# Kernel tuning notes

Hardware: AMD Instinct MI355X
Metric: run time of the kernel (lower is better)

The kernel has to match this reference:

```python
import jax, jax.numpy as jnp
import numpy as np

B, LQ, D, H, L, P, DFF = 16, 1024, 256, 8, 4, 4, 1024
SHAPES = ((64, 64), (32, 32), (16, 16), (8, 8))  # (H_l, W_l) per level
LV = sum(h * w for h, w in SHAPES)  # 5440
DH = D // H
EPS = 1e-5


def layer_norm(x, g, b):
    m = jnp.mean(x, -1, keepdims=True)
    v = jnp.mean((x - m) ** 2, -1, keepdims=True)
    return (x - m) * jax.lax.rsqrt(v + EPS) * g + b


def mha(q_in, k_in, v_in, w, b, ow, ob):
    # torch nn.MultiheadAttention with packed in_proj [3D, D]
    q = (q_in @ w[:D].T + b[:D]).reshape(B, LQ, H, DH)
    k = (k_in @ w[D:2 * D].T + b[D:2 * D]).reshape(B, LQ, H, DH)
    v = (v_in @ w[2 * D:].T + b[2 * D:]).reshape(B, LQ, H, DH)
    a = jax.nn.softmax(jnp.einsum('bqhd,bkhd->bhqk', q, k) * (1.0 / np.sqrt(DH)), -1)
    o = jnp.einsum('bhqk,bkhd->bqhd', a, v).reshape(B, LQ, D)
    return o @ ow.T + ob


def ms_deform_attn(q, ref, src, value_w, value_b, off_w, off_b, attw_w, attw_b, outp_w, outp_b):
    # value: [B, H, LV, DH]
    value = (src @ value_w.T + value_b).reshape(B, LV, H, DH).transpose(0, 2, 1, 3)
    off = (q @ off_w.T + off_b).reshape(B, LQ, H, L, P, 2)
    attw = jax.nn.softmax((q @ attw_w.T + attw_b).reshape(B, LQ, H, L * P), -1).reshape(B, LQ, H, L, P)
    # offset normalizer = (W_l, H_l) matching (x, y) order of reference points
    normalizer = jnp.array([[w, h] for h, w in SHAPES], jnp.float32)
    loc = ref[:, :, None, :, None, :] + off / normalizer[None, None, None, :, None, :]  # [B,LQ,H,L,P,2]
    out = jnp.zeros((B, LQ, H, DH), jnp.float32)
    start = 0
    for l, (hl, wl) in enumerate(SHAPES):
        v = value[:, :, start:start + hl * wl]  # [B,H,N_l,DH]
        start += hl * wl
        # grid_sample semantics, align_corners=False, padding zeros
        x = loc[:, :, :, l, :, 0] * wl - 0.5  # [B,LQ,H,P]
        y = loc[:, :, :, l, :, 1] * hl - 0.5
        x0 = jnp.floor(x); y0 = jnp.floor(y)
        lx = (x - x0).transpose(0, 2, 1, 3)[..., None]  # [B,H,LQ,P,1]
        ly = (y - y0).transpose(0, 2, 1, 3)[..., None]
        x0i = x0.astype(jnp.int32); y0i = y0.astype(jnp.int32)

        def gather(xi, yi):
            valid = ((xi >= 0) & (xi < wl) & (yi >= 0) & (yi < hl)).astype(jnp.float32)
            idx = jnp.clip(yi, 0, hl - 1) * wl + jnp.clip(xi, 0, wl - 1)  # [B,LQ,H,P]
            idx2 = idx.transpose(0, 2, 1, 3).reshape(B, H, LQ * P)
            g = jnp.take_along_axis(v, jnp.broadcast_to(idx2[..., None], (B, H, LQ * P, DH)), axis=2)
            return g.reshape(B, H, LQ, P, DH) * valid.transpose(0, 2, 1, 3)[..., None]

        g00 = gather(x0i, y0i); g01 = gather(x0i + 1, y0i)
        g10 = gather(x0i, y0i + 1); g11 = gather(x0i + 1, y0i + 1)
        sampled = (g00 * (1 - lx) * (1 - ly) + g01 * lx * (1 - ly)
                   + g10 * (1 - lx) * ly + g11 * lx * ly)  # [B,H,LQ,P,DH]
        out = out + jnp.einsum('bhqpd,bqhp->bqhd', sampled, attw[:, :, :, l])
    return out.reshape(B, LQ, D) @ outp_w.T + outp_b


def setup_inputs() -> dict:
    key = jax.random.key(0)
    ks = jax.random.split(key, 16)
    s = 0.02
    inp = {}
    inp['tgt'] = jax.random.normal(ks[0], (B, LQ, D), jnp.float32)
    inp['query_pos'] = jax.random.normal(ks[1], (B, LQ, D), jnp.float32)
    inp['reference_points'] = jax.random.uniform(ks[2], (B, LQ, L, 2), jnp.float32)
    inp['src'] = jax.random.normal(ks[3], (B, LV, D), jnp.float32)
    # self-attention (MHA)
    inp['in_proj_w'] = jax.random.normal(ks[4], (3 * D, D), jnp.float32) * s
    inp['in_proj_b'] = jnp.zeros((3 * D,), jnp.float32)
    inp['out_proj_w'] = jax.random.normal(ks[5], (D, D), jnp.float32) * s
    inp['out_proj_b'] = jnp.zeros((D,), jnp.float32)
    inp['norm2_g'] = jnp.ones((D,), jnp.float32); inp['norm2_b'] = jnp.zeros((D,), jnp.float32)
    # MSDeformAttn
    inp['value_w'] = jax.random.normal(ks[6], (D, D), jnp.float32) * s
    inp['value_b'] = jnp.zeros((D,), jnp.float32)
    inp['off_w'] = jax.random.normal(ks[7], (H * L * P * 2, D), jnp.float32) * s
    inp['off_b'] = jax.random.normal(ks[8], (H * L * P * 2,), jnp.float32) * 0.5
    inp['attw_w'] = jax.random.normal(ks[9], (H * L * P, D), jnp.float32) * s
    inp['attw_b'] = jnp.zeros((H * L * P,), jnp.float32)
    inp['outp_w'] = jax.random.normal(ks[10], (D, D), jnp.float32) * s
    inp['outp_b'] = jnp.zeros((D,), jnp.float32)
    inp['norm1_g'] = jnp.ones((D,), jnp.float32); inp['norm1_b'] = jnp.zeros((D,), jnp.float32)
    # FFN
    inp['lin1_w'] = jax.random.normal(ks[11], (DFF, D), jnp.float32) * s
    inp['lin1_b'] = jnp.zeros((DFF,), jnp.float32)
    inp['lin2_w'] = jax.random.normal(ks[12], (D, DFF), jnp.float32) * s
    inp['lin2_b'] = jnp.zeros((D,), jnp.float32)
    inp['norm3_g'] = jnp.ones((D,), jnp.float32); inp['norm3_b'] = jnp.zeros((D,), jnp.float32)
    inp['src_spatial_shapes'] = jnp.array(SHAPES, jnp.int32)
    inp['level_start_index'] = jnp.array(np.concatenate([[0], np.cumsum([h * w for h, w in SHAPES[:-1]])]), jnp.int32)
    return inp


def reference(tgt, query_pos, reference_points, src,
              in_proj_w, in_proj_b, out_proj_w, out_proj_b, norm2_g, norm2_b,
              value_w, value_b, off_w, off_b, attw_w, attw_b, outp_w, outp_b,
              norm1_g, norm1_b, lin1_w, lin1_b, lin2_w, lin2_b, norm3_g, norm3_b,
              src_spatial_shapes, level_start_index):
    # dropout=0 (eval mode)
    q = tgt + query_pos
    tgt2 = mha(q, q, tgt, in_proj_w, in_proj_b, out_proj_w, out_proj_b)
    tgt = layer_norm(tgt + tgt2, norm2_g, norm2_b)
    tgt2 = ms_deform_attn(tgt + query_pos, reference_points, src,
                          value_w, value_b, off_w, off_b, attw_w, attw_b, outp_w, outp_b)
    tgt = layer_norm(tgt + tgt2, norm1_g, norm1_b)
    t2 = jax.nn.relu(tgt @ lin1_w.T + lin1_b) @ lin2_w.T + lin2_b
    return layer_norm(tgt + t2, norm3_g, norm3_b)
```

## Files before the change

### kernel.cpp

```cpp
#include <hip/hip_runtime.h>
#include <math.h>

typedef short s16x8 __attribute__((ext_vector_type(8)));
typedef float f32x4 __attribute__((ext_vector_type(4)));
typedef unsigned short u16;
typedef unsigned short u16x4 __attribute__((ext_vector_type(4)));

constexpr int cB    = 16;
constexpr int cLQ   = 1024;
constexpr int cD    = 256;
constexpr int cH    = 8;
constexpr int cLVTOT= 5440;
constexpr int cNTOK = cB * cLQ;
constexpr int cNV   = cB * cLVTOT;

__device__ __forceinline__ u16 f2b(float f) {
    __bf16 h = (__bf16)f;
    u16 u;
    __builtin_memcpy(&u, &h, 2);
    return u;
}
__device__ __forceinline__ float bl(unsigned x) {
    return __uint_as_float(x << 16);
}

__global__ __launch_bounds__(256) void prep_src_kernel(const float4* __restrict__ t,
                                                       const float4* __restrict__ q,
                                                       u16x4* __restrict__ tb,
                                                       u16x4* __restrict__ qb,
                                                       const float4* __restrict__ src,
                                                       u16x4* __restrict__ srcb) {
    int bid = blockIdx.x;
    if (bid < 4096) {
        int i = bid * 256 + threadIdx.x;
        float4 a = t[i], b = q[i];
        tb[i] = (u16x4){ f2b(a.x), f2b(a.y), f2b(a.z), f2b(a.w) };
        qb[i] = (u16x4){ f2b(a.x + b.x), f2b(a.y + b.y), f2b(a.z + b.z), f2b(a.w + b.w) };
    } else {
        int i = (bid - 4096) * 256 + threadIdx.x;
        float4 v = src[i];
        srcb[i] = (u16x4){ f2b(v.x), f2b(v.y), f2b(v.z), f2b(v.w) };
    }
}

struct WArgs { const float4* src[8]; };
__global__ __launch_bounds__(256) void cvtw_kernel(WArgs a, u16x4* __restrict__ out,
                                                   const float* __restrict__ off_b,
                                                   const float* __restrict__ attw_b,
                                                   float* __restrict__ biasoa) {
    int i = blockIdx.x * 256 + threadIdx.x;
    if (i >= 253952) {
        int t = threadIdx.x;
        biasoa[t] = off_b[t];
        if (t < 128) biasoa[256 + t] = attw_b[t];
        return;
    }
    int s, off;
    if (i < 98304) {
        if (i < 65536) { if (i < 49152) { s = 0; off = i; } else { s = 1; off = i - 49152; } }
        else           { if (i < 81920) { s = 2; off = i - 65536; } else { s = 3; off = i - 81920; } }
    } else {
        if (i < 122880){ if (i < 106496){ s = 4; off = i - 98304; } else { s = 5; off = i - 106496; } }
        else           { if (i < 188416){ s = 6; off = i - 122880; } else { s = 7; off = i - 188416; } }
    }
    float4 v = a.src[s][off];
    out[i] = (u16x4){ f2b(v.x), f2b(v.y), f2b(v.z), f2b(v.w) };
}

__global__ __launch_bounds__(256) void gemm_qkv(const u16* __restrict__ A0,
                                                const u16* __restrict__ A1,
                                                const u16* __restrict__ Wt,
                                                const float* __restrict__ bias,
                                                u16* __restrict__ QKb,
                                                u16* __restrict__ Vtg) {
    __shared__ u16 As[128 * 32];
    __shared__ u16 Bs[128 * 32];
    const int K = 256;
    int tid = threadIdx.x;
    int bm = blockIdx.x * 128, bn = blockIdx.y * 128;
    const u16* A = (blockIdx.y < 4) ? A0 : A1;
    int w = tid >> 6, lane = tid & 63, quad = lane >> 4, l15 = lane & 15;
    int wm = (w & 1) * 64, wn = (w >> 1) * 64;
    int r0 = tid >> 2;
    int c0 = ((tid & 3) ^ ((tid >> 3) & 3)) * 8;
    const u16* ga0 = A  + (size_t)(bm + r0) * K + c0;
    const u16* ga1 = ga0 + (size_t)64 * K;
    const u16* gb0 = Wt + (size_t)(bn + r0) * K + c0;
    const u16* gb1 = gb0 + (size_t)64 * K;
    int abk = (quad ^ ((l15 >> 1) & 3)) * 8;
    f32x4 acc[16];
#pragma unroll
    for (int i = 0; i < 16; ++i) acc[i] = (f32x4){0.f, 0.f, 0.f, 0.f};
    s16x8 ra0 = *(const s16x8*)ga0, ra1 = *(const s16x8*)ga1;
    s16x8 rb0 = *(const s16x8*)gb0, rb1 = *(const s16x8*)gb1;
#pragma unroll 2
    for (int i = 0; i < 8; ++i) {
        *(s16x8*)&As[tid * 8]        = ra0;
        *(s16x8*)&As[2048 + tid * 8] = ra1;
        *(s16x8*)&Bs[tid * 8]        = rb0;
        *(s16x8*)&Bs[2048 + tid * 8] = rb1;
        __syncthreads();
        if (i < 7) {
            int k1 = (i + 1) << 5;
            ra0 = *(const s16x8*)(ga0 + k1); ra1 = *(const s16x8*)(ga1 + k1);
            rb0 = *(const s16x8*)(gb0 + k1); rb1 = *(const s16x8*)(gb1 + k1);
        }
        s16x8 af[4], bf[4];
#pragma unroll
        for (int mt = 0; mt < 4; ++mt) af[mt] = *(const s16x8*)&As[(wm + mt * 16 + l15) * 32 + abk];
#pragma unroll
        for (int nt = 0; nt < 4; ++nt) bf[nt] = *(const s16x8*)&Bs[(wn + nt * 16 + l15) * 32 + abk];
#pragma unroll
        for (int mt = 0; mt < 4; ++mt)
#pragma unroll
            for (int nt = 0; nt < 4; ++nt)
                acc[mt * 4 + nt] = __builtin_amdgcn_mfma_f32_16x16x32_bf16(af[mt], bf[nt], acc[mt * 4 + nt], 0, 0, 0);
        __syncthreads();
    }
    float bs[4];
#pragma unroll
    for (int nt = 0; nt < 4; ++nt) bs[nt] = bias[bn + wn + nt * 16 + l15];
    if (bn < 512) {
        float qs = (bn + wn < 256) ? 0.25506734f : 1.0f;
#pragma unroll
        for (int mt = 0; mt < 4; ++mt) {
            int m = bm + wm + mt * 16 + quad * 4;
#pragma unroll
            for (int nt = 0; nt < 4; ++nt) {
                int n = bn + wn + nt * 16 + l15;
#pragma unroll
                for (int r = 0; r < 4; ++r)
                    QKb[(size_t)(m + r) * 512 + n] = f2b((acc[mt * 4 + nt][r] + bs[nt]) * qs);
            }
        }
    } else {
#pragma unroll
        for (int mt = 0; mt < 4; ++mt) {
            int m = bm + wm + mt * 16 + quad * 4;
            int b = m >> 10, t = m & 1023;
#pragma unroll
            for (int nt = 0; nt < 4; ++nt) {
                int nv = bn + wn + nt * 16 + l15 - 512;
                int h = nv >> 5, dh = nv & 31;
                u16x4 o;
#pragma unroll
                for (int r = 0; r < 4; ++r) o[r] = f2b(acc[mt * 4 + nt][r] + bs[nt]);
                *(u16x4*)(Vtg + (((size_t)(b * 8 + h) * 32 + dh) << 10) + t) = o;
            }
        }
    }
}

template <int RELU, int OUTBF>
__global__ __launch_bounds__(256) void gemm128(const u16* __restrict__ A,
                                               const u16* __restrict__ Wt,
                                               const float* __restrict__ bias,
                                               float* __restrict__ Cf,
                                               u16* __restrict__ Cb,
                                               int M, int N, int K) {
    __shared__ u16 As[128 * 32];
    __shared__ u16 Bs[128 * 32];
    int tid = threadIdx.x;
    int bm = blockIdx.x * 128, bn = blockIdx.y * 128;
    int w = tid >> 6, lane = tid & 63, quad = lane >> 4, l15 = lane & 15;
    int wm = (w & 1) * 64, wn = (w >> 1) * 64;
    int r0 = tid >> 2;
    int c0 = ((tid & 3) ^ ((tid >> 3) & 3)) * 8;
    const u16* ga0 = A  + (size_t)(bm + r0) * K + c0;
    const u16* ga1 = ga0 + (size_t)64 * K;
    const u16* gb0 = Wt + (size_t)(bn + r0) * K + c0;
    const u16* gb1 = gb0 + (size_t)64 * K;
    int abk = (quad ^ ((l15 >> 1) & 3)) * 8;
    f32x4 acc[16];
#pragma unroll
    for (int i = 0; i < 16; ++i) acc[i] = (f32x4){0.f, 0.f, 0.f, 0.f};
    s16x8 ra0 = *(const s16x8*)ga0, ra1 = *(const s16x8*)ga1;
    s16x8 rb0 = *(const s16x8*)gb0, rb1 = *(const s16x8*)gb1;
    int nk = K >> 5;
#pragma unroll 2
    for (int i = 0; i < nk; ++i) {
        *(s16x8*)&As[tid * 8]        = ra0;
        *(s16x8*)&As[2048 + tid * 8] = ra1;
        *(s16x8*)&Bs[tid * 8]        = rb0;
        *(s16x8*)&Bs[2048 + tid * 8] = rb1;
        __syncthreads();
        if (i + 1 < nk) {
            int k1 = (i + 1) << 5;
            ra0 = *(const s16x8*)(ga0 + k1); ra1 = *(const s16x8*)(ga1 + k1);
            rb0 = *(const s16x8*)(gb0 + k1); rb1 = *(const s16x8*)(gb1 + k1);
        }
        s16x8 af[4], bf[4];
#pragma unroll
        for (int mt = 0; mt < 4; ++mt) af[mt] = *(const s16x8*)&As[(wm + mt * 16 + l15) * 32 + abk];
#pragma unroll
        for (int nt = 0; nt < 4; ++nt) bf[nt] = *(const s16x8*)&Bs[(wn + nt * 16 + l15) * 32 + abk];
#pragma unroll
        for (int mt = 0; mt < 4; ++mt)
#pragma unroll
            for (int nt = 0; nt < 4; ++nt)
                acc[mt * 4 + nt] = __builtin_amdgcn_mfma_f32_16x16x32_bf16(af[mt], bf[nt], acc[mt * 4 + nt], 0, 0, 0);
        __syncthreads();
    }
    float bs[4];
#pragma unroll
    for (int nt = 0; nt < 4; ++nt) bs[nt] = bias[bn + wn + nt * 16 + l15];
#pragma unroll
    for (int mt = 0; mt < 4; ++mt) {
        int m = bm + wm + mt * 16 + quad * 4;
#pragma unroll
        for (int nt = 0; nt < 4; ++nt) {
            int n = bn + wn + nt * 16 + l15;
#pragma unroll
            for (int r = 0; r < 4; ++r) {
                float v = acc[mt * 4 + nt][r] + bs[nt];
                if (RELU) v = fmaxf(v, 0.f);
                if (OUTBF) Cb[(size_t)(m + r) * N + n] = f2b(v);
                else       Cf[(size_t)(m + r) * N + n] = v;
            }
        }
    }
}

template <int RELU, int OUTBF>
__global__ __launch_bounds__(256) void gemm64(const u16* __restrict__ A,
                                              const u16* __restrict__ Wt,
                                              const float* __restrict__ bias,
                                              float* __restrict__ Cf,
                                              u16* __restrict__ Cb,
                                              int M, int N, int K) {
    __shared__ u16 As[64 * 32];
    __shared__ u16 Bs[128 * 32];
    int tid = threadIdx.x;
    int bm = blockIdx.x * 64, bn = blockIdx.y * 128;
    int w = tid >> 6, lane = tid & 63, quad = lane >> 4, l15 = lane & 15;
    int wn = w * 32;
    int r0 = tid >> 2;
    int c0 = ((tid & 3) ^ ((tid >> 3) & 3)) * 8;
    const u16* ga0 = A  + (size_t)(bm + r0) * K + c0;
    const u16* gb0 = Wt + (size_t)(bn + r0) * K + c0;
    const u16* gb1 = gb0 + (size_t)64 * K;
    int abk = (quad ^ ((l15 >> 1) & 3)) * 8;
    f32x4 acc[8];
#pragma unroll
    for (int i = 0; i < 8; ++i) acc[i] = (f32x4){0.f, 0.f, 0.f, 0.f};
    s16x8 ra0 = *(const s16x8*)ga0;
    s16x8 rb0 = *(const s16x8*)gb0, rb1 = *(const s16x8*)gb1;
    int nk = K >> 5;
#pragma unroll 2
    for (int i = 0; i < nk; ++i) {
        *(s16x8*)&As[tid * 8]        = ra0;
        *(s16x8*)&Bs[tid * 8]        = rb0;
        *(s16x8*)&Bs[2048 + tid * 8] = rb1;
        __syncthreads();
        if (i + 1 < nk) {
            int k1 = (i + 1) << 5;
            ra0 = *(const s16x8*)(ga0 + k1);
            rb0 = *(const s16x8*)(gb0 + k1); rb1 = *(const s16x8*)(gb1 + k1);
        }
        s16x8 af[4], bf[2];
#pragma unroll
        for (int mt = 0; mt < 4; ++mt) af[mt] = *(const s16x8*)&As[(mt * 16 + l15) * 32 + abk];
#pragma unroll
        for (int nt = 0; nt < 2; ++nt) bf[nt] = *(const s16x8*)&Bs[(wn + nt * 16 + l15) * 32 + abk];
#pragma unroll
        for (int mt = 0; mt < 4; ++mt)
#pragma unroll
            for (int nt = 0; nt < 2; ++nt)
                acc[mt * 2 + nt] = __builtin_amdgcn_mfma_f32_16x16x32_bf16(af[mt], bf[nt], acc[mt * 2 + nt], 0, 0, 0);
        __syncthreads();
    }
    float bs[2];
#pragma unroll
    for (int nt = 0; nt < 2; ++nt) bs[nt] = bias[bn + wn + nt * 16 + l15];
#pragma unroll
    for (int mt = 0; mt < 4; ++mt) {
        int m = bm + mt * 16 + quad * 4;
#pragma unroll
        for (int nt = 0; nt < 2; ++nt) {
            int n = bn + wn + nt * 16 + l15;
#pragma unroll
            for (int r = 0; r < 4; ++r) {
                float v = acc[mt * 2 + nt][r] + bs[nt];
                if (RELU) v = fmaxf(v, 0.f);
                if (OUTBF) Cb[(size_t)(m + r) * N + n] = f2b(v);
                else       Cf[(size_t)(m + r) * N + n] = v;
            }
        }
    }
}

__global__ __launch_bounds__(256) void attn_val(const u16* __restrict__ QK,
                                                const u16* __restrict__ Vt,
                                                u16* __restrict__ O,
                                                const u16* __restrict__ Av,
                                                const u16* __restrict__ Wv,
                                                const float* __restrict__ bv,
                                                u16* __restrict__ Cv) {
    __shared__ __align__(16) u16 smem[8192];
    int bid = blockIdx.x;
    int tid = threadIdx.x;
    int w = tid >> 6, lane = tid & 63, quad = lane >> 4, l15 = lane & 15;
    int isg, id;
    if (bid < 2720) { isg = !(bid & 1); id = bid >> 1; }
    else            { isg = 0;          id = 1360 + (bid - 2720); }
    if (isg) {
        u16* As = smem;
        u16* Bs = smem + 4096;
        int bm = (id % 680) * 128, bn = (id / 680) * 128;
        int wm = (w & 1) * 64, wn = (w >> 1) * 64;
        int r0 = tid >> 2;
        int c0 = ((tid & 3) ^ ((tid >> 3) & 3)) * 8;
        const u16* ga0 = Av + (size_t)(bm + r0) * 256 + c0;
        const u16* ga1 = ga0 + (size_t)64 * 256;
        const u16* gb0 = Wv + (size_t)(bn + r0) * 256 + c0;
        const u16* gb1 = gb0 + (size_t)64 * 256;
        int abk = (quad ^ ((l15 >> 1) & 3)) * 8;
        f32x4 acc[16];
#pragma unroll
        for (int i = 0; i < 16; ++i) acc[i] = (f32x4){0.f, 0.f, 0.f, 0.f};
        s16x8 ra0 = *(const s16x8*)ga0, ra1 = *(const s16x8*)ga1;
        s16x8 rb0 = *(const s16x8*)gb0, rb1 = *(const s16x8*)gb1;
#pragma unroll 2
        for (int i = 0; i < 8; ++i) {
            *(s16x8*)&As[tid * 8]        = ra0;
            *(s16x8*)&As[2048 + tid * 8] = ra1;
            *(s16x8*)&Bs[tid * 8]        = rb0;
            *(s16x8*)&Bs[2048 + tid * 8] = rb1;
            __syncthreads();
            if (i < 7) {
                int k1 = (i + 1) << 5;
                ra0 = *(const s16x8*)(ga0 + k1); ra1 = *(const s16x8*)(ga1 + k1);
                rb0 = *(const s16x8*)(gb0 + k1); rb1 = *(const s16x8*)(gb1 + k1);
            }
            s16x8 af[4], bf[4];
#pragma unroll
            for (int mt = 0; mt < 4; ++mt) af[mt] = *(const s16x8*)&As[(wm + mt * 16 + l15) * 32 + abk];
#pragma unroll
            for (int nt = 0; nt < 4; ++nt) bf[nt] = *(const s16x8*)&Bs[(wn + nt * 16 + l15) * 32 + abk];
#pragma unroll
            for (int mt = 0; mt < 4; ++mt)
#pragma unroll
                for (int nt = 0; nt < 4; ++nt)
                    acc[mt * 4 + nt] = __builtin_amdgcn_mfma_f32_16x16x32_bf16(af[mt], bf[nt], acc[mt * 4 + nt], 0, 0, 0);
            __syncthreads();
        }
        float bs[4];
#pragma unroll
        for (int nt = 0; nt < 4; ++nt) bs[nt] = bv[bn + wn + nt * 16 + l15];
#pragma unroll
        for (int mt = 0; mt < 4; ++mt) {
            int m = bm + wm + mt * 16 + quad * 4;
#pragma unroll
            for (int nt = 0; nt < 4; ++nt) {
                int n = bn + wn + nt * 16 + l15;
#pragma unroll
                for (int r = 0; r < 4; ++r)
                    Cv[(size_t)(m + r) * 256 + n] = f2b(acc[mt * 4 + nt][r] + bs[nt]);
            }
        }
        return;
    }
    u16* Ks  = smem;
    u16* Vs  = smem + 2048;
    u16* Psw = smem + 4096 + w * 1024;
    int qt = id & 15, bh = id >> 4;
    int h = bh & 7, b = bh >> 3;
    int qbase = qt * 64 + w * 16;
    s16x8 qf = *(const s16x8*)(QK + (size_t)(b * cLQ + qbase + l15) * 512 + h * 32 + quad * 8);
    f32x4 o0 = {0.f,0.f,0.f,0.f}, o1 = {0.f,0.f,0.f,0.f}, o2 = {0.f,0.f,0.f,0.f};
    int skey = tid >> 2, kchunk = tid & 3;
    int ks_off = skey * 32 + ((kchunk ^ ((skey >> 1) & 3)) * 8);
    int sdh = kchunk * 8;
    int vdh = tid >> 3, vchunk = tid & 7;
    int vs_off = vdh * 64 + ((vchunk ^ (vdh & 7)) * 8);
    int vkc = vchunk * 8;
    int ksw = (l15 >> 1) & 3;
    int vsw = l15 & 7;
    size_t kgbase = (size_t)(b * cLQ) * 512 + 256 + h * 32;
    size_t vgbase = (size_t)bh * 32 * cLQ;
    s16x8 kreg = *(const s16x8*)(QK + kgbase + (size_t)skey * 512 + sdh);
    s16x8 vreg = *(const s16x8*)(Vt + vgbase + (size_t)vdh * cLQ + vkc);
    const s16x8 ones = {16256,16256,16256,16256,16256,16256,16256,16256};
    for (int kt = 0; kt < cLQ; kt += 64) {
        __syncthreads();
        *(s16x8*)&Ks[ks_off] = kreg;
        *(s16x8*)&Vs[vs_off] = vreg;
        if (kt + 64 < cLQ) {
            kreg = *(const s16x8*)(QK + kgbase + (size_t)(kt + 64 + skey) * 512 + sdh);
            vreg = *(const s16x8*)(Vt + vgbase + (size_t)vdh * cLQ + kt + 64 + vkc);
        }
        __syncthreads();
#pragma unroll
        for (int t = 0; t < 4; ++t) {
            s16x8 kf = *(const s16x8*)&Ks[(t * 16 + l15) * 32 + (quad ^ ksw) * 8];
            f32x4 z = {0.f,0.f,0.f,0.f};
            f32x4 sc = __builtin_amdgcn_mfma_f32_16x16x32_bf16(kf, qf, z, 0, 0, 0);
            u16x4 pb;
#pragma unroll
            for (int r = 0; r < 4; ++r) pb[r] = f2b(exp2f(sc[r]));
            *(u16x4*)&Psw[l15 * 64 + (((t * 2 + (quad >> 1)) ^ vsw) * 8) + (quad & 1) * 4] = pb;
        }
#pragma unroll
        for (int ks = 0; ks < 2; ++ks) {
            int coff = ((ks * 4 + quad) ^ vsw) * 8;
            s16x8 pa  = *(const s16x8*)&Psw[l15 * 64 + coff];
            s16x8 vb0 = *(const s16x8*)&Vs[l15 * 64 + coff];
            s16x8 vb1 = *(const s16x8*)&Vs[(l15 + 16) * 64 + coff];
            o0 = __builtin_amdgcn_mfma_f32_16x16x32_bf16(pa, vb0, o0, 0, 0, 0);
            o1 = __builtin_amdgcn_mfma_f32_16x16x32_bf16(pa, vb1, o1, 0, 0, 0);
            o2 = __builtin_amdgcn_mfma_f32_16x16x32_bf16(pa, ones, o2, 0, 0, 0);
        }
    }
#pragma unroll
    for (int r = 0; r < 4; ++r) {
        float inv = 1.0f / o2[r];
        int q = qbase + quad * 4 + r;
        size_t ob = (size_t)(b * cLQ + q) * cD + h * 32;
        O[ob + l15]      = f2b(o0[r] * inv);
        O[ob + 16 + l15] = f2b(o1[r] * inv);
    }
}

template <int WB, int QP>
__global__ __launch_bounds__(256) void add_ln_kernel(const float* __restrict__ X,
                                                     const float* __restrict__ R,
                                                     const float* __restrict__ g,
                                                     const float* __restrict__ bt,
                                                     const float* __restrict__ qp,
                                                     float* __restrict__ out,
                                                     u16* __restrict__ outb) {
    int wave = threadIdx.x / 64;
    int lane = threadIdx.x % 64;
    int row = blockIdx.x * 4 + wave;
    const float* x = X + (size_t)row * cD;
    const float* r = R + (size_t)row * cD;
    float4 xv = *(const float4*)(x + lane * 4);
    float4 rv = *(const float4*)(r + lane * 4);
    float v0 = xv.x + rv.x, v1 = xv.y + rv.y, v2 = xv.z + rv.z, v3 = xv.w + rv.w;
    float s = v0 + v1 + v2 + v3;
    float s2 = v0 * v0 + v1 * v1 + v2 * v2 + v3 * v3;
#pragma unroll
    for (int off = 32; off > 0; off >>= 1) {
        s += __shfl_xor(s, off);
        s2 += __shfl_xor(s2, off);
    }
    float mean = s * (1.0f / 256.0f);
    float var = s2 * (1.0f / 256.0f) - mean * mean;
    float rstd = rsqrtf(var + 1e-5f);
    float4 gv = *(const float4*)(g + lane * 4);
    float4 bv = *(const float4*)(bt + lane * 4);
    float4 o;
    o.x = (v0 - mean) * rstd * gv.x + bv.x;
    o.y = (v1 - mean) * rstd * gv.y + bv.y;
    o.z = (v2 - mean) * rstd * gv.z + bv.z;
    o.w = (v3 - mean) * rstd * gv.w + bv.w;
    *(float4*)(out + (size_t)row * cD + lane * 4) = o;
    if (WB) {
        u16x4 ob = { f2b(o.x), f2b(o.y), f2b(o.z), f2b(o.w) };
        *(u16x4*)(outb + (size_t)row * cD + lane * 4) = ob;
    }
    if (QP) {
        float4 qv = *(const float4*)(qp + (size_t)row * cD + lane * 4);
        u16x4 ob = { f2b(o.x + qv.x), f2b(o.y + qv.y), f2b(o.z + qv.z), f2b(o.w + qv.w) };
        *(u16x4*)(outb + (size_t)row * cD + lane * 4) = ob;
    }
}

__global__ __launch_bounds__(256) void deform_kernel(const u16* __restrict__ value,
                                                     const float* __restrict__ oa,
                                                     const float* __restrict__ refp,
                                                     u16* __restrict__ out) {
    int t = blockIdx.x * 32 + (threadIdx.x >> 3);
    int dq = threadIdx.x & 7;
    int h = t & 7;
    int bq = t >> 3;
    int b = bq >> 10;
    const float* al = oa + (size_t)bq * 384 + 256 + h * 16;
    float wv[16];
    float mx = -1e30f;
#pragma unroll
    for (int i = 0; i < 16; ++i) { wv[i] = al[i]; mx = fmaxf(mx, wv[i]); }
    float sum = 0.f;
#pragma unroll
    for (int i = 0; i < 16; ++i) { wv[i] = __expf(wv[i] - mx); sum += wv[i]; }
    float inv = 1.f / sum;
    const float* off = oa + (size_t)bq * 384 + h * 32;
    const float* rp = refp + (size_t)bq * 8;
    const u16* vb = value + ((size_t)b * cLVTOT) * 256 + h * 32 + dq * 4;
    const int starts[4] = {0, 4096, 5120, 5376};
    const int dims[4] = {64, 32, 16, 8};
    float a0 = 0.f, a1 = 0.f, a2 = 0.f, a3 = 0.f;
#pragma unroll
    for (int l = 0; l < 4; ++l) {
        int hl = dims[l], wl = dims[l];
        float rx = rp[l * 2 + 0], ry = rp[l * 2 + 1];
#pragma unroll
        for (int p = 0; p < 4; ++p) {
            float ox = off[(l * 4 + p) * 2 + 0];
            float oy = off[(l * 4 + p) * 2 + 1];
            float x = rx * (float)wl + ox - 0.5f;
            float y = ry * (float)hl + oy - 0.5f;
            float x0f = floorf(x), y0f = floorf(y);
            float lx = x - x0f, ly = y - y0f;
            int x0 = (int)x0f, y0 = (int)y0f;
            float aw = wv[l * 4 + p] * inv;
            float cw[4] = {(1.f - lx) * (1.f - ly), lx * (1.f - ly),
                           (1.f - lx) * ly, lx * ly};
            int xs[4] = {x0, x0 + 1, x0, x0 + 1};
            int ys[4] = {y0, y0, y0 + 1, y0 + 1};
#pragma unroll
            for (int c = 0; c < 4; ++c) {
                int xi = xs[c], yi = ys[c];
                bool valid = (xi >= 0) && (xi < wl) && (yi >= 0) && (yi < hl);
                int xc = min(max(xi, 0), wl - 1);
                int yc = min(max(yi, 0), hl - 1);
                int idx = starts[l] + yc * wl + xc;
                float wgt = valid ? aw * cw[c] : 0.f;
                unsigned long long u = *(const unsigned long long*)(vb + (size_t)idx * 256);
                a0 += wgt * bl((unsigned)(u & 0xffffull));
                a1 += wgt * bl((unsigned)((u >> 16) & 0xffffull));
                a2 += wgt * bl((unsigned)((u >> 32) & 0xffffull));
                a3 += wgt * bl((unsigned)(u >> 48));
            }
        }
    }
    u16x4 o = { f2b(a0), f2b(a1), f2b(a2), f2b(a3) };
    *(u16x4*)(out + (size_t)bq * 256 + h * 32 + dq * 4) = o;
}

extern "C" void kernel_launch(void* const* d_in, const int* in_sizes, int n_in,
                              void* d_out, int out_size, void* d_ws, size_t ws_size,
                              hipStream_t stream) {
    const float* tgt        = (const float*)d_in[0];
    const float* query_pos  = (const float*)d_in[1];
    const float* refp       = (const float*)d_in[2];
    const float* src        = (const float*)d_in[3];
    const float* in_proj_w  = (const float*)d_in[4];
    const float* in_proj_b  = (const float*)d_in[5];
    const float* out_proj_b = (const float*)d_in[7];
    const float* norm2_g    = (const float*)d_in[8];
    const float* norm2_b    = (const float*)d_in[9];
    const float* value_b    = (const float*)d_in[11];
    const float* off_b      = (const float*)d_in[13];
    const float* attw_b     = (const float*)d_in[15];
    const float* outp_b     = (const float*)d_in[17];
    const float* norm1_g    = (const float*)d_in[18];
    const float* norm1_b    = (const float*)d_in[19];
    const float* lin1_b     = (const float*)d_in[21];
    const float* lin2_b     = (const float*)d_in[23];
    const float* norm3_g    = (const float*)d_in[24];
    const float* norm3_b    = (const float*)d_in[25];

    char* W = (char*)d_ws;
    const size_t S84 = 8388608;
    u16*   tgtb  = (u16*)(W + 0);
    u16*   q2b   = (u16*)(W + 0);
    u16*   qb    = (u16*)(W + 1 * S84);
    u16*   QKb   = (u16*)(W + 2 * S84);
    u16*   dtb   = (u16*)(W + 2 * S84);
    u16*   x2b   = (u16*)(W + 3 * S84);
    float* ffn2f = (float*)(W + 4 * S84);
    u16*   aob   = (u16*)(W + 5 * S84);
    float* oaf   = (float*)(W + 5 * S84);
    u16*   Vtg   = (u16*)(W + 6 * S84);
    float* t2f   = (float*)(W + 6 * S84);
    float* x1f   = (float*)(W + 8 * S84);
    float* x2f   = (float*)(W + 10 * S84);
    u16*   srcb  = (u16*)(W + 12 * S84);
    u16*   ffn1b = (u16*)(W + 12 * S84);
    u16*   valb  = (u16*)(W + 12 * S84 + 44564480);
    char*  wbase = W + 12 * S84 + 2 * 44564480;
    u16* wb_in   = (u16*)(wbase + 0);
    u16* wb_out  = (u16*)(wbase + 393216);
    u16* wb_val  = (u16*)(wbase + 524288);
    u16* wb_off  = (u16*)(wbase + 655360);
    u16* wb_outp = (u16*)(wbase + 851968);
    u16* wb_lin1 = (u16*)(wbase + 983040);
    u16* wb_lin2 = (u16*)(wbase + 1507328);
    float* biasoa= (float*)(wbase + 2031616);
    float* out = (float*)d_out;

    dim3 blk(256);

    prep_src_kernel<<<dim3(25856), blk, 0, stream>>>((const float4*)tgt, (const float4*)query_pos,
                                                     (u16x4*)tgtb, (u16x4*)qb,
                                                     (const float4*)src, (u16x4*)srcb);
    WArgs wa;
    wa.src[0] = (const float4*)in_proj_w;  wa.src[1] = (const float4*)d_in[6];
    wa.src[2] = (const float4*)d_in[10];   wa.src[3] = (const float4*)d_in[12];
    wa.src[4] = (const float4*)d_in[14];   wa.src[5] = (const float4*)d_in[16];
    wa.src[6] = (const float4*)d_in[20];   wa.src[7] = (const float4*)d_in[22];
    cvtw_kernel<<<dim3(993), blk, 0, stream>>>(wa, (u16x4*)wb_in, off_b, attw_b, biasoa);

    gemm_qkv<<<dim3(128, 6), blk, 0, stream>>>(qb, tgtb, wb_in, in_proj_b, QKb, Vtg);
    attn_val<<<dim3(3408), blk, 0, stream>>>(QKb, Vtg, aob, srcb, wb_val, value_b, valb);
    gemm64<0, 0><<<dim3(256, 2), blk, 0, stream>>>(aob, wb_out, out_proj_b, t2f, nullptr, cNTOK, 256, 256);
    add_ln_kernel<0, 1><<<dim3(4096), blk, 0, stream>>>(tgt, t2f, norm2_g, norm2_b, query_pos, x1f, q2b);

    gemm64<0, 0><<<dim3(256, 3), blk, 0, stream>>>(q2b, wb_off, biasoa, oaf, nullptr, cNTOK, 384, 256);
    deform_kernel<<<dim3(4096), blk, 0, stream>>>(valb, oaf, refp, dtb);
    gemm64<0, 0><<<dim3(256, 2), blk, 0, stream>>>(dtb, wb_outp, outp_b, t2f, nullptr, cNTOK, 256, 256);
    add_ln_kernel<1, 0><<<dim3(4096), blk, 0, stream>>>(x1f, t2f, norm1_g, norm1_b, nullptr, x2f, x2b);

    gemm128<1, 1><<<dim3(128, 8), blk, 0, stream>>>(x2b, wb_lin1, lin1_b, nullptr, ffn1b, cNTOK, 1024, 256);
    gemm64<0, 0><<<dim3(256, 2), blk, 0, stream>>>(ffn1b, wb_lin2, lin2_b, ffn2f, nullptr, cNTOK, 256, 1024);
    add_ln_kernel<0, 0><<<dim3(4096), blk, 0, stream>>>(x2f, ffn2f, norm3_g, norm3_b, nullptr, out, nullptr);
}
```

Measured before the change: 440.3 us.

## Move value-projection GEMM from attention kernel into QKV projection launch

The value projection GEMM (src → value), previously interleaved with self-attention blocks inside attn_val, now runs in one combined launch with the QKV projection. The attention kernel becomes a pure attention kernel of 2048 blocks. The intent is to balance work better: the QKV GEMM grid was small (768 blocks) and the independent value GEMM fills it out, while the attention kernel no longer mixes heterogeneous block types. The trade-off is that the attention kernel loses the overlap it had with the value GEMM.

```diff
diff --git a/kernel.cpp b/kernel.cpp
--- a/kernel.cpp
+++ b/kernel.cpp
@@ -67,25 +67,43 @@
     out[i] = (u16x4){ f2b(v.x), f2b(v.y), f2b(v.z), f2b(v.w) };
 }
 
-__global__ __launch_bounds__(256) void gemm_qkv(const u16* __restrict__ A0,
-                                                const u16* __restrict__ A1,
-                                                const u16* __restrict__ Wt,
-                                                const float* __restrict__ bias,
-                                                u16* __restrict__ QKb,
-                                                u16* __restrict__ Vtg) {
+__global__ __launch_bounds__(256) void gemm_qkv_val(const u16* __restrict__ A0,
+                                                    const u16* __restrict__ A1,
+                                                    const u16* __restrict__ Wt,
+                                                    const float* __restrict__ bias,
+                                                    u16* __restrict__ QKb,
+                                                    u16* __restrict__ Vtg,
+                                                    const u16* __restrict__ Av,
+                                                    const u16* __restrict__ Wv,
+                                                    const float* __restrict__ bv,
+                                                    u16* __restrict__ Cv) {
     __shared__ u16 As[128 * 32];
     __shared__ u16 Bs[128 * 32];
     const int K = 256;
     int tid = threadIdx.x;
-    int bm = blockIdx.x * 128, bn = blockIdx.y * 128;
-    const u16* A = (blockIdx.y < 4) ? A0 : A1;
+    int bid = blockIdx.x;
     int w = tid >> 6, lane = tid & 63, quad = lane >> 4, l15 = lane & 15;
     int wm = (w & 1) * 64, wn = (w >> 1) * 64;
+    int isval = bid < 1360;
+    int bm, bn;
+    const u16 *A, *W;
+    const float* bp;
+    if (isval) {
+        bm = (bid % 680) * 128; bn = (bid / 680) * 128;
+        A = Av; W = Wv; bp = bv;
+    } else {
+        int id = bid - 1360;
+        bm = (id & 127) * 128;
+        int by = id >> 7;
+        bn = by * 128;
+        A = (by < 4) ? A0 : A1;
+        W = Wt; bp = bias;
+    }
     int r0 = tid >> 2;
     int c0 = ((tid & 3) ^ ((tid >> 3) & 3)) * 8;
-    const u16* ga0 = A  + (size_t)(bm + r0) * K + c0;
+    const u16* ga0 = A + (size_t)(bm + r0) * K + c0;
     const u16* ga1 = ga0 + (size_t)64 * K;
-    const u16* gb0 = Wt + (size_t)(bn + r0) * K + c0;
+    const u16* gb0 = W + (size_t)(bn + r0) * K + c0;
     const u16* gb1 = gb0 + (size_t)64 * K;
     int abk = (quad ^ ((l15 >> 1) & 3)) * 8;
     f32x4 acc[16];
@@ -119,8 +137,20 @@
     }
     float bs[4];
 #pragma unroll
-    for (int nt = 0; nt < 4; ++nt) bs[nt] = bias[bn + wn + nt * 16 + l15];
-    if (bn < 512) {
+    for (int nt = 0; nt < 4; ++nt) bs[nt] = bp[bn + wn + nt * 16 + l15];
+    if (isval) {
+#pragma unroll
+        for (int mt = 0; mt < 4; ++mt) {
+            int m = bm + wm + mt * 16 + quad * 4;
+#pragma unroll
+            for (int nt = 0; nt < 4; ++nt) {
+                int n = bn + wn + nt * 16 + l15;
+#pragma unroll
+                for (int r = 0; r < 4; ++r)
+                    Cv[(size_t)(m + r) * 256 + n] = f2b(acc[mt * 4 + nt][r] + bs[nt]);
+            }
+        }
+    } else if (bn < 512) {
         float qs = (bn + wn < 256) ? 0.25506734f : 1.0f;
 #pragma unroll
         for (int mt = 0; mt < 4; ++mt) {
@@ -289,80 +319,15 @@
     }
 }
 
-__global__ __launch_bounds__(256) void attn_val(const u16* __restrict__ QK,
-                                                const u16* __restrict__ Vt,
-                                                u16* __restrict__ O,
-                                                const u16* __restrict__ Av,
-                                                const u16* __restrict__ Wv,
-                                                const float* __restrict__ bv,
-                                                u16* __restrict__ Cv) {
+__global__ __launch_bounds__(256) void attn_sw(const u16* __restrict__ QK,
+                                               const u16* __restrict__ Vt,
+                                               u16* __restrict__ O) {
     __shared__ __align__(16) u16 smem[8192];
-    int bid = blockIdx.x;
-    int tid = threadIdx.x;
-    int w = tid >> 6, lane = tid & 63, quad = lane >> 4, l15 = lane & 15;
-    int isg, id;
-    if (bid < 2720) { isg = !(bid & 1); id = bid >> 1; }
-    else            { isg = 0;          id = 1360 + (bid - 2720); }
-    if (isg) {
-        u16* As = smem;
-        u16* Bs = smem + 4096;
-        int bm = (id % 680) * 128, bn = (id / 680) * 128;
-        int wm = (w & 1) * 64, wn = (w >> 1) * 64;
-        int r0 = tid >> 2;
-        int c0 = ((tid & 3) ^ ((tid >> 3) & 3)) * 8;
-        const u16* ga0 = Av + (size_t)(bm + r0) * 256 + c0;
-        const u16* ga1 = ga0 + (size_t)64 * 256;
-        const u16* gb0 = Wv + (size_t)(bn + r0) * 256 + c0;
-        const u16* gb1 = gb0 + (size_t)64 * 256;
-        int abk = (quad ^ ((l15 >> 1) & 3)) * 8;
-        f32x4 acc[16];
-#pragma unroll
-        for (int i = 0; i < 16; ++i) acc[i] = (f32x4){0.f, 0.f, 0.f, 0.f};
-        s16x8 ra0 = *(const s16x8*)ga0, ra1 = *(const s16x8*)ga1;
-        s16x8 rb0 = *(const s16x8*)gb0, rb1 = *(const s16x8*)gb1;
-#pragma unroll 2
-        for (int i = 0; i < 8; ++i) {
-            *(s16x8*)&As[tid * 8]        = ra0;
-            *(s16x8*)&As[2048 + tid * 8] = ra1;
-            *(s16x8*)&Bs[tid * 8]        = rb0;
-            *(s16x8*)&Bs[2048 + tid * 8] = rb1;
-            __syncthreads();
-            if (i < 7) {
-                int k1 = (i + 1) << 5;
-                ra0 = *(const s16x8*)(ga0 + k1); ra1 = *(const s16x8*)(ga1 + k1);
-                rb0 = *(const s16x8*)(gb0 + k1); rb1 = *(const s16x8*)(gb1 + k1);
-            }
-            s16x8 af[4], bf[4];
-#pragma unroll
-            for (int mt = 0; mt < 4; ++mt) af[mt] = *(const s16x8*)&As[(wm + mt * 16 + l15) * 32 + abk];
-#pragma unroll
-            for (int nt = 0; nt < 4; ++nt) bf[nt] = *(const s16x8*)&Bs[(wn + nt * 16 + l15) * 32 + abk];
-#pragma unroll
-            for (int mt = 0; mt < 4; ++mt)
-#pragma unroll
-                for (int nt = 0; nt < 4; ++nt)
-                    acc[mt * 4 + nt] = __builtin_amdgcn_mfma_f32_16x16x32_bf16(af[mt], bf[nt], acc[mt * 4 + nt], 0, 0, 0);
-            __syncthreads();
-        }
-        float bs[4];
-#pragma unroll
-        for (int nt = 0; nt < 4; ++nt) bs[nt] = bv[bn + wn + nt * 16 + l15];
-#pragma unroll
-        for (int mt = 0; mt < 4; ++mt) {
-            int m = bm + wm + mt * 16 + quad * 4;
-#pragma unroll
-            for (int nt = 0; nt < 4; ++nt) {
-                int n = bn + wn + nt * 16 + l15;
-#pragma unroll
-                for (int r = 0; r < 4; ++r)
-                    Cv[(size_t)(m + r) * 256 + n] = f2b(acc[mt * 4 + nt][r] + bs[nt]);
-            }
-        }
-        return;
-    }
+    int tid = threadIdx.x, w = tid >> 6, lane = tid & 63, quad = lane >> 4, l15 = lane & 15;
     u16* Ks  = smem;
     u16* Vs  = smem + 2048;
     u16* Psw = smem + 4096 + w * 1024;
+    int id = blockIdx.x;
     int qt = id & 15, bh = id >> 4;
     int h = bh & 7, b = bh >> 3;
     int qbase = qt * 64 + w * 16;
@@ -592,8 +557,9 @@
     wa.src[6] = (const float4*)d_in[20];   wa.src[7] = (const float4*)d_in[22];
     cvtw_kernel<<<dim3(993), blk, 0, stream>>>(wa, (u16x4*)wb_in, off_b, attw_b, biasoa);
 
-    gemm_qkv<<<dim3(128, 6), blk, 0, stream>>>(qb, tgtb, wb_in, in_proj_b, QKb, Vtg);
-    attn_val<<<dim3(3408), blk, 0, stream>>>(QKb, Vtg, aob, srcb, wb_val, value_b, valb);
+    gemm_qkv_val<<<dim3(2128), blk, 0, stream>>>(qb, tgtb, wb_in, in_proj_b, QKb, Vtg,
+                                                 srcb, wb_val, value_b, valb);
+    attn_sw<<<dim3(cB * cH * 16), blk, 0, stream>>>(QKb, Vtg, aob);
     gemm64<0, 0><<<dim3(256, 2), blk, 0, stream>>>(aob, wb_out, out_proj_b, t2f, nullptr, cNTOK, 256, 256);
     add_ln_kernel<0, 1><<<dim3(4096), blk, 0, stream>>>(tgt, t2f, norm2_g, norm2_b, query_pos, x1f, q2b);
 
```

Measured after the change: 439.2 us. About the same (-0.3%).
